# Performance work log

Measured on AMD Instinct MI355X. Metric: run time of the kernel, lower is better.

Reference implementation:

```python
import jax, jax.numpy as jnp
from jax import lax
import numpy as np


def _conv3d(x, W, b, stride=1, pad=1):
    y = lax.conv_general_dilated(x, W, (stride,) * 3, [(pad, pad)] * 3,
                                 dimension_numbers=('NCDHW', 'OIDHW', 'NCDHW'))
    return y + b[None, :, None, None, None]


def _deconv3d(x, W, b):
    # PyTorch ConvTranspose3d(k=4, s=2, p=1) == conv with lhs_dilation=2,
    # per-side pad = k-1-p = 2, spatially flipped kernel; W is (Cin, Cout, 4,4,4).
    Wf = jnp.flip(W, axis=(2, 3, 4)).transpose(1, 0, 2, 3, 4)
    y = lax.conv_general_dilated(x, Wf, (1, 1, 1), [(2, 2)] * 3,
                                 lhs_dilation=(2, 2, 2),
                                 dimension_numbers=('NCDHW', 'OIDHW', 'NCDHW'))
    return y + b[None, :, None, None, None]


def _inorm(x, eps=1e-5):
    # InstanceNorm3d (affine=False): normalize per (B, C) over spatial dims
    m = jnp.mean(x, axis=(2, 3, 4), keepdims=True)
    v = jnp.var(x, axis=(2, 3, 4), keepdims=True)
    return (x - m) * lax.rsqrt(v + eps)


def _leaky(x):
    return jnp.where(x >= 0, x, 0.1 * x)


def _cblock(x, W, b, stride=1):
    return _leaky(_inorm(_conv3d(x, W, b, stride)))


def _cost_volume(f1, f2, r=2):
    # Faithful to the original pad/mul/crop loop:
    # cost[shift][p] = mean_c f1[c, p] * f2[c, p + shift], zero-padded OOB.
    B, C, D, H, W = f1.shape
    f2p = jnp.pad(f2, ((0, 0), (0, 0), (r, r), (r, r), (r, r)))
    cv = [jnp.mean(f1 * f2p[:, :, r + v:r + v + D, r + h:r + h + H, r + d:r + d + W], axis=1)
          for v in range(-r, r + 1)
          for h in range(-r, r + 1)
          for d in range(-r, r + 1)]
    return jnp.stack(cv, axis=1)  # (B, (2r+1)^3 = 125, D, H, W)


def _warp(img, flow):
    # SpatialTransformation: dense 3D warp, trilinear sample at grid + flow,
    # coordinates clamped to the volume border.
    B, C, D, H, W = img.shape
    gd, gh, gw = jnp.meshgrid(jnp.arange(D, dtype=img.dtype),
                              jnp.arange(H, dtype=img.dtype),
                              jnp.arange(W, dtype=img.dtype), indexing='ij')
    cd = jnp.clip(gd[None] + flow[:, 0], 0.0, D - 1.0)
    ch = jnp.clip(gh[None] + flow[:, 1], 0.0, H - 1.0)
    cw = jnp.clip(gw[None] + flow[:, 2], 0.0, W - 1.0)

    def samp_b(imb, d, h, w):
        return jax.vmap(lambda c: jax.scipy.ndimage.map_coordinates(
            c, [d, h, w], order=1, mode='nearest'))(imb)

    return jax.vmap(samp_b)(img, cd, ch, cw)


def _forward(atlas, target, W_ct, b_ct, W1a, b1a, W1aa, b1aa, W1b, b1b,
             W2a, b2a, W2aa, b2aa, W2b, b2b,
             W20, b20, Wpf2, bpf2, Wd2, bd2, Wuf2, buf2,
             W10, b10, Wpf1, bpf1, Wd1, bd1, Wuf1, buf1,
             W00, b00, Wpf0, bpf0, Wd0, bd0):
    # modality='CT' (shared CT encoder), G=True, contrastive=False path
    im2 = _cblock(atlas, W_ct, b_ct, stride=2)
    im1 = _cblock(target, W_ct, b_ct, stride=2)
    c11 = _cblock(_cblock(_cblock(im1, W1a, b1a, 2), W1aa, b1aa), W1b, b1b)
    c21 = _cblock(_cblock(_cblock(im2, W1a, b1a, 2), W1aa, b1aa), W1b, b1b)
    c12 = _cblock(_cblock(_cblock(c11, W2a, b2a, 2), W2aa, b2aa), W2b, b2b)
    c22 = _cblock(_cblock(_cblock(c21, W2a, b2a, 2), W2aa, b2aa), W2b, b2b)

    x = _leaky(_cost_volume(c12, c22))
    x = _cblock(x, W20, b20)
    flow2 = _conv3d(x, Wpf2, bpf2)
    up_flow2 = _deconv3d(flow2, Wd2, bd2)
    up_feat2 = _deconv3d(x, Wuf2, buf2)

    warp1 = _warp(c21, up_flow2)
    corr1 = _leaky(_cost_volume(c11, warp1))
    x = jnp.concatenate((corr1, c11, up_flow2, up_feat2), axis=1)  # 125+16+3+3=147
    x = _cblock(x, W10, b10)
    flow1 = _conv3d(x, Wpf1, bpf1)
    up_flow1 = _deconv3d(flow1, Wd1, bd1)
    up_feat1 = _deconv3d(x, Wuf1, buf1)

    warp0 = _warp(im2, up_flow1)
    corr0 = _leaky(_cost_volume(im1, warp0))
    x = jnp.concatenate((corr0, im1, up_flow1, up_feat1), axis=1)  # 125+4+3+64=196
    x = _cblock(x, W00, b00)
    flow0 = _conv3d(x, Wpf0, bpf0)
    flow = _deconv3d(flow0, Wd0, bd0)
    return flow, c22, c12


def setup_inputs() -> dict:
    ks = jax.random.split(jax.random.key(0), 24)

    def w(i, shape):
        fan_in = int(np.prod(shape[1:]))
        return jax.random.normal(ks[i], shape, jnp.float32) * np.float32(np.sqrt(2.0 / fan_in))

    z = lambda n: jnp.zeros((n,), jnp.float32)
    S = 128
    return {
        'atlas': jax.random.normal(ks[0], (1, 1, S, S, S), jnp.float32),
        'target': jax.random.normal(ks[1], (1, 1, S, S, S), jnp.float32),
        'W_ct': w(2, (4, 1, 3, 3, 3)), 'b_ct': z(4),
        'W1a': w(3, (16, 4, 3, 3, 3)), 'b1a': z(16),
        'W1aa': w(4, (16, 16, 3, 3, 3)), 'b1aa': z(16),
        'W1b': w(5, (16, 16, 3, 3, 3)), 'b1b': z(16),
        'W2a': w(6, (32, 16, 3, 3, 3)), 'b2a': z(32),
        'W2aa': w(7, (32, 32, 3, 3, 3)), 'b2aa': z(32),
        'W2b': w(8, (32, 32, 3, 3, 3)), 'b2b': z(32),
        'W20': w(9, (32, 125, 3, 3, 3)), 'b20': z(32),
        'Wpf2': w(10, (3, 32, 3, 3, 3)) * 0.1, 'bpf2': z(3),
        'Wd2': w(11, (3, 3, 4, 4, 4)), 'bd2': z(3),
        'Wuf2': w(12, (32, 3, 4, 4, 4)), 'buf2': z(3),
        'W10': w(13, (32, 147, 3, 3, 3)), 'b10': z(32),
        'Wpf1': w(14, (3, 32, 3, 3, 3)) * 0.1, 'bpf1': z(3),
        'Wd1': w(15, (3, 3, 4, 4, 4)), 'bd1': z(3),
        'Wuf1': w(16, (32, 64, 4, 4, 4)), 'buf1': z(64),
        'W00': w(17, (32, 196, 3, 3, 3)), 'b00': z(32),
        'Wpf0': w(18, (3, 32, 3, 3, 3)) * 0.1, 'bpf0': z(3),
        'Wd0': w(19, (3, 3, 4, 4, 4)), 'bd0': z(3),
    }


def reference(atlas, target, W_ct, b_ct, W1a, b1a, W1aa, b1aa, W1b, b1b,
              W2a, b2a, W2aa, b2aa, W2b, b2b,
              W20, b20, Wpf2, bpf2, Wd2, bd2, Wuf2, buf2,
              W10, b10, Wpf1, bpf1, Wd1, bd1, Wuf1, buf1,
              W00, b00, Wpf0, bpf0, Wd0, bd0):
    return _forward(atlas, target, W_ct, b_ct, W1a, b1a, W1aa, b1aa, W1b, b1b,
                    W2a, b2a, W2aa, b2aa, W2b, b2b,
                    W20, b20, Wpf2, bpf2, Wd2, bd2, Wuf2, buf2,
                    W10, b10, Wpf1, bpf1, Wd1, bd1, Wuf1, buf1,
                    W00, b00, Wpf0, bpf0, Wd0, bd0)
```

## Files before the change

kernel.cpp:

```cpp
#include <hip/hip_runtime.h>
#include <cstddef>
#include <cstdint>

#define DIVUP(a,b) (((a)+(b)-1)/(b))

typedef __attribute__((ext_vector_type(8))) short short8;
typedef __attribute__((ext_vector_type(4))) float f32x4;

__device__ __forceinline__ ushort f2bf(float f) {
    union { float f; uint32_t u; } v; v.f = f;
    uint32_t r = v.u + 0x7fffu + ((v.u >> 16) & 1u);
    return (ushort)(r >> 16);
}

struct SwzB { int x, y, z; };
__device__ __forceinline__ SwzB swz_block() {
    int gx = gridDim.x, gy = gridDim.y;
    int n = gx * gy * gridDim.z;
    int lin = blockIdx.x + gx * (blockIdx.y + gy * blockIdx.z);
    if ((n & 7) == 0)
        lin = (lin & 7) * (n >> 3) + (lin >> 3);
    SwzB s;
    s.x = lin % gx;
    int t = lin / gx;
    s.y = t % gy;
    s.z = t / gy;
    return s;
}

template<int COUT, int STRIDE>
__global__ __launch_bounds__(256)
void conv3x3_k(const float* __restrict__ in0, const float* __restrict__ in1,
               const float* __restrict__ wgt, const float* __restrict__ bias,
               float* __restrict__ out, float* __restrict__ stats,
               int Cin, int D, int H, int W, int nz, long out_bs, int st_bs)
{
    constexpr int TD = 4, TH = 8, TW = 8;
    constexpr int ID = 2 * TD + 1, IH = 2 * TH + 1, IW = 2 * TW + 1;
    __shared__ float tile[ID * IH * IW];
    const int b = blockIdx.z / nz, zb = blockIdx.z % nz;
    const float* in = b ? in1 : in0;
    out += (long)b * out_bs;
    if (stats) stats += 2 * st_bs * b;
    const int Do = D / STRIDE, Ho = H / STRIDE, Wo = W / STRIDE;
    const int tid = threadIdx.x;
    const int tw = tid & 7, th = (tid >> 3) & 7, td = tid >> 6;
    const int ow0 = blockIdx.x * TW, oh0 = blockIdx.y * TH, od0 = zb * TD;
    const int iw0 = ow0 * STRIDE - 1, ih0 = oh0 * STRIDE - 1, id0 = od0 * STRIDE - 1;
    const size_t HWs = (size_t)H * W;

    float acc[COUT];
#pragma unroll
    for (int i = 0; i < COUT; i++) acc[i] = 0.f;

    for (int c = 0; c < Cin; ++c) {
        const float* inc = in + (size_t)c * D * HWs;
        for (int i = tid; i < ID * IH * IW; i += 256) {
            int lw = i % IW, lh = (i / IW) % IH, ld = i / (IW * IH);
            int gw = iw0 + lw, gh = ih0 + lh, gd = id0 + ld;
            float v = 0.f;
            if ((unsigned)gw < (unsigned)W && (unsigned)gh < (unsigned)H &&
                (unsigned)gd < (unsigned)D)
                v = inc[(size_t)gd * HWs + (size_t)gh * W + gw];
            tile[i] = v;
        }
        __syncthreads();
        float r[27];
        const int bd = td * STRIDE, bh = th * STRIDE, bw = tw * STRIDE;
#pragma unroll
        for (int kd = 0; kd < 3; kd++)
#pragma unroll
            for (int kh = 0; kh < 3; kh++)
#pragma unroll
                for (int kw = 0; kw < 3; kw++)
                    r[kd * 9 + kh * 3 + kw] =
                        tile[(bd + kd) * (IH * IW) + (bh + kh) * IW + (bw + kw)];
#pragma unroll
        for (int oc = 0; oc < COUT; ++oc) {
            const float* wp = wgt + ((size_t)oc * Cin + c) * 27;
            float s = 0.f;
#pragma unroll
            for (int t = 0; t < 27; t++) s = fmaf(wp[t], r[t], s);
            acc[oc] += s;
        }
        __syncthreads();
    }
    const size_t So = (size_t)Do * Ho * Wo;
    const size_t sp = (size_t)(od0 + td) * Ho * Wo + (size_t)(oh0 + th) * Wo + (ow0 + tw);
#pragma unroll
    for (int oc = 0; oc < COUT; ++oc)
        out[(size_t)oc * So + sp] = acc[oc] + bias[oc];

    if (stats) {
        __syncthreads();
        float* sm = tile;
        const int wv = tid >> 6, l = tid & 63;
#pragma unroll
        for (int oc = 0; oc < COUT; ++oc) {
            float sv = acc[oc] + bias[oc];
            float sq = sv * sv;
#pragma unroll
            for (int o = 32; o > 0; o >>= 1) {
                sv += __shfl_down(sv, o, 64);
                sq += __shfl_down(sq, o, 64);
            }
            if (l == 0) { sm[(wv * COUT + oc) * 2] = sv; sm[(wv * COUT + oc) * 2 + 1] = sq; }
        }
        __syncthreads();
        if (tid < COUT) {
            float s = 0.f, s2 = 0.f;
#pragma unroll
            for (int w = 0; w < 4; ++w) {
                s += sm[(w * COUT + tid) * 2];
                s2 += sm[(w * COUT + tid) * 2 + 1];
            }
            atomicAdd(&stats[2 * tid], s);
            atomicAdd(&stats[2 * tid + 1], s2);
        }
    }
}

template<int CP, int NF, int STRIDE, int MW, int COUTR>
__global__ __launch_bounds__(MW * 64, (STRIDE == 1 && MW == 4) ? 2 : 4)
void mconv_k(const ushort* __restrict__ xcl, const ushort* __restrict__ wp,
             const float* __restrict__ bias, float* __restrict__ outcf,
             float* __restrict__ stats, const ushort* __restrict__ zbuf,
             int D, int H, int W, int nz, long in_bs, long out_bs, int st_bs)
{
    constexpr int KC = CP / 32;
    constexpr int MF = (STRIDE == 1) ? 4 : 1;
    constexpr int TD = MW;
    constexpr int TWl = (STRIDE == 1) ? 8 : 4;
    constexpr int HD = (STRIDE == 1) ? TD + 2 : 2 * TD + 1;
    constexpr int HH = (STRIDE == 1) ? 10 : 9;
    constexpr int HWd = (STRIDE == 1) ? 10 : 9;
    constexpr int HALO = HD * HH * HWd;
    constexpr int NTH = MW * 64;
    constexpr int NIT = (HALO * 4 + NTH - 1) / NTH;
    constexpr int PITCH = (STRIDE == 1) ? 32 : 40;
    constexpr bool WLDS = (STRIDE == 1 && MW == 4);
    constexpr int LDSZ_H = (STRIDE == 1) ? NIT * NTH * 8 : HALO * 40;
    constexpr int NITW = (9 * NF * 512 + NTH * 8 - 1) / (NTH * 8);
    constexpr int LDSZ_W = NITW * NTH * 8;
    constexpr int LDS_TOT = WLDS ? LDSZ_H + 2 * LDSZ_W : LDSZ_H;
    __shared__ __align__(16) ushort lds[LDS_TOT];

    const int tid = threadIdx.x;
    const int wv = tid >> 6, l = tid & 63;
    const SwzB sb = swz_block();
    const int b = sb.z / nz, zb = sb.z % nz;
    xcl += (long)b * in_bs;
    outcf += (long)b * out_bs;
    if (stats) stats += 2 * st_bs * b;
    const int od0 = zb * TD, oh0 = sb.y * ((STRIDE == 1) ? 8 : 4),
              ow0 = sb.x * TWl;
    const int id0 = od0 * STRIDE - 1, ih0 = oh0 * STRIDE - 1, iw0 = ow0 * STRIDE - 1;

    f32x4 acc[MF][NF];
#pragma unroll
    for (int mf = 0; mf < MF; mf++)
#pragma unroll
        for (int nf = 0; nf < NF; nf++) acc[mf][nf] = f32x4{0.f, 0.f, 0.f, 0.f};

    auto woff = [&](int kc, int kd, int kh, int kw, int nf) -> size_t {
        return ((((size_t)(kc * 3 + kd) * 3 + kh) * 3 + kw) * NF + nf) << 9;
    };

    if constexpr (WLDS) {
        ushort* const hab = lds;
        ushort* const wbA = lds + LDSZ_H;
        ushort* const wbB = lds + LDSZ_H + LDSZ_W;

        auto hstage = [&](int kc) {
#pragma unroll
            for (int it = 0; it < NIT; ++it) {
                int idx = it * NTH + tid;
                int pt = idx >> 2, part = idx & 3;
                int lw = pt % HWd, lh = (pt / HWd) % HH, ld = pt / (HWd * HH);
                int gx = iw0 + lw, gy = ih0 + lh, gz = id0 + ld;
                const ushort* src = zbuf;
                if (pt < HALO && (unsigned)gx < (unsigned)W &&
                    (unsigned)gy < (unsigned)H && (unsigned)gz < (unsigned)D)
                    src = xcl + (size_t)((gz * H + gy) * W + gx) * CP + part * 8;
                __builtin_amdgcn_global_load_lds(
                    (const __attribute__((address_space(1))) uint32_t*)(src + kc * 32),
                    (__attribute__((address_space(3))) uint32_t*)
                        &hab[(size_t)(it * NTH + (wv << 6)) * 8],
                    16, 0, 0);
            }
        };
        auto wstage = [&](int kc, int kd, ushort* dst) {
#pragma unroll
            for (int it = 0; it < NITW; ++it) {
                int idx = it * NTH + tid;
                const ushort* src = (idx < 9 * NF * 64)
                    ? wp + ((size_t)(kc * 3 + kd) * 9 * NF * 512 + (size_t)idx * 8)
                    : zbuf;
                __builtin_amdgcn_global_load_lds(
                    (const __attribute__((address_space(1))) uint32_t*)src,
                    (__attribute__((address_space(3))) uint32_t*)
                        &dst[(size_t)(it * NTH + (wv << 6)) * 8],
                    16, 0, 0);
            }
        };
        auto compute = [&](int kd, const ushort* w) {
#pragma unroll
            for (int kw = 0; kw < 3; ++kw) {
                short8 af[9];
#pragma unroll
                for (int r = 0; r < 9; ++r)
                    af[r] = *reinterpret_cast<const short8*>(
                        &hab[((wv + kd) * (HH * HWd) +
                              (r + ((l >> 3) & 1)) * HWd + (l & 7) + kw) * PITCH +
                             ((l >> 4) << 3)]);
#pragma unroll
                for (int kh = 0; kh < 3; ++kh) {
                    short8 bf[NF];
#pragma unroll
                    for (int nf = 0; nf < NF; ++nf)
                        bf[nf] = *reinterpret_cast<const short8*>(
                            &w[(size_t)(((kh * 3 + kw) * NF) + nf) * 512 + (l << 3)]);
#pragma unroll
                    for (int mf = 0; mf < MF; ++mf)
#pragma unroll
                        for (int nf = 0; nf < NF; ++nf)
                            acc[mf][nf] = __builtin_amdgcn_mfma_f32_16x16x32_bf16(
                                af[2 * mf + kh], bf[nf], acc[mf][nf], 0, 0, 0);
                }
            }
        };

        for (int kc = 0; kc < KC; ++kc) {
            hstage(kc);
            wstage(kc, 0, wbA);
            __syncthreads();
            wstage(kc, 1, wbB);
            compute(0, wbA);
            __syncthreads();
            wstage(kc, 2, wbA);
            compute(1, wbB);
            __syncthreads();
            compute(2, wbA);
            __syncthreads();
        }
    } else if constexpr (STRIDE == 1) {
        for (int kc = 0; kc < KC; ++kc) {
            if (kc) __syncthreads();
#pragma unroll
            for (int it = 0; it < NIT; ++it) {
                int idx = it * NTH + tid;
                int pt = idx >> 2, part = idx & 3;
                int lw = pt % HWd, lh = (pt / HWd) % HH, ld = pt / (HWd * HH);
                int gx = iw0 + lw, gy = ih0 + lh, gz = id0 + ld;
                const ushort* src = zbuf;
                if (pt < HALO && (unsigned)gx < (unsigned)W &&
                    (unsigned)gy < (unsigned)H && (unsigned)gz < (unsigned)D)
                    src = xcl + (size_t)((gz * H + gy) * W + gx) * CP + part * 8;
                __builtin_amdgcn_global_load_lds(
                    (const __attribute__((address_space(1))) uint32_t*)(src + kc * 32),
                    (__attribute__((address_space(3))) uint32_t*)
                        &lds[(size_t)(it * NTH + (wv << 6)) * 8],
                    16, 0, 0);
            }
            __syncthreads();
#pragma unroll
            for (int kd = 0; kd < 3; ++kd) {
#pragma unroll
                for (int kw = 0; kw < 3; ++kw) {
                    short8 af[9];
#pragma unroll
                    for (int r = 0; r < 9; ++r)
                        af[r] = *reinterpret_cast<const short8*>(
                            &lds[((wv + kd) * (HH * HWd) +
                                  (r + ((l >> 3) & 1)) * HWd + (l & 7) + kw) * PITCH +
                                 ((l >> 4) << 3)]);
#pragma unroll
                    for (int kh = 0; kh < 3; ++kh) {
                        short8 bf[NF];
#pragma unroll
                        for (int nf = 0; nf < NF; ++nf)
                            bf[nf] = *reinterpret_cast<const short8*>(
                                wp + woff(kc, kd, kh, kw, nf) + (l << 3));
#pragma unroll
                        for (int mf = 0; mf < MF; ++mf)
#pragma unroll
                            for (int nf = 0; nf < NF; ++nf)
                                acc[mf][nf] = __builtin_amdgcn_mfma_f32_16x16x32_bf16(
                                    af[2 * mf + kh], bf[nf], acc[mf][nf], 0, 0, 0);
                    }
                }
            }
        }
    } else {
        uint4 v[NIT];
        auto stage = [&](int kc) {
#pragma unroll
            for (int it = 0; it < NIT; ++it) {
                int idx = it * NTH + tid;
                uint4 t = {0u, 0u, 0u, 0u};
                if (idx < HALO * 4) {
                    int pt = idx >> 2, part = idx & 3;
                    int lw = pt % HWd, lh = (pt / HWd) % HH, ld = pt / (HWd * HH);
                    int gx = iw0 + lw, gy = ih0 + lh, gz = id0 + ld;
                    if ((unsigned)gx < (unsigned)W && (unsigned)gy < (unsigned)H &&
                        (unsigned)gz < (unsigned)D)
                        t = *reinterpret_cast<const uint4*>(
                            xcl + ((size_t)((gz * H + gy) * W + gx)) * CP + kc * 32 + part * 8);
                }
                v[it] = t;
            }
        };

        stage(0);
        for (int kc = 0; kc < KC; ++kc) {
            if (kc) __syncthreads();
#pragma unroll
            for (int it = 0; it < NIT; ++it) {
                int idx = it * NTH + tid;
                if (idx < HALO * 4)
                    *reinterpret_cast<uint4*>(&lds[(idx >> 2) * PITCH + (idx & 3) * 8]) = v[it];
            }
            __syncthreads();
            if (kc + 1 < KC) stage(kc + 1);
#pragma unroll
            for (int t = 0; t < 27; ++t) {
                const int kd = t / 9, kh = (t / 3) % 3, kw = t % 3;
                short8 bf[NF];
#pragma unroll
                for (int nf = 0; nf < NF; ++nf)
                    bf[nf] = *reinterpret_cast<const short8*>(
                        wp + woff(kc, kd, kh, kw, nf) + (l << 3));
                int bw = l & 3, bh = (l >> 2) & 3;
                int p_loc = (2 * wv + kd) * (HH * HWd) + (2 * bh + kh) * HWd + (2 * bw + kw);
                short8 afs = *reinterpret_cast<const short8*>(&lds[p_loc * PITCH + ((l >> 4) << 3)]);
#pragma unroll
                for (int nf = 0; nf < NF; ++nf)
                    acc[0][nf] = __builtin_amdgcn_mfma_f32_16x16x32_bf16(
                        afs, bf[nf], acc[0][nf], 0, 0, 0);
            }
        }
    }
    const int Do = D / STRIDE, Ho = H / STRIDE, Wo = W / STRIDE;
    const size_t So = (size_t)Do * Ho * Wo;
    float ps[NF], ps2[NF];
#pragma unroll
    for (int nf = 0; nf < NF; ++nf) { ps[nf] = 0.f; ps2[nf] = 0.f; }
#pragma unroll
    for (int nf = 0; nf < NF; ++nf) {
        int oc = nf * 16 + (l & 15);
        float bv = (oc < COUTR) ? bias[oc] : 0.f;
#pragma unroll
        for (int mf = 0; mf < MF; ++mf) {
#pragma unroll
            for (int r = 0; r < 4; ++r) {
                int q = ((l >> 4) << 2) + r;
                int bw, bh;
                if (STRIDE == 1) { bw = q & 7; bh = 2 * mf + (q >> 3); }
                else             { bw = q & 3; bh = (q >> 2) & 3; }
                int p = ((od0 + wv) * Ho + (oh0 + bh)) * Wo + (ow0 + bw);
                float val = acc[mf][nf][r] + bv;
                if (oc < COUTR) {
                    outcf[(size_t)oc * So + p] = val;
                    ps[nf] += val; ps2[nf] = fmaf(val, val, ps2[nf]);
                }
            }
        }
    }
    if (stats) {
        __syncthreads();
        float* sm = (float*)lds;
#pragma unroll
        for (int nf = 0; nf < NF; ++nf) {
            float s = ps[nf], s2 = ps2[nf];
            s += __shfl_down(s, 32, 64);  s2 += __shfl_down(s2, 32, 64);
            s += __shfl_down(s, 16, 64);  s2 += __shfl_down(s2, 16, 64);
            if (l < 16) {
                sm[((wv * NF + nf) * 16 + l) * 2] = s;
                sm[((wv * NF + nf) * 16 + l) * 2 + 1] = s2;
            }
        }
        __syncthreads();
        if (tid < NF * 16) {
            int nf = tid >> 4, c = tid & 15, oc = nf * 16 + c;
            if (oc < COUTR) {
                float s = 0.f, s2 = 0.f;
#pragma unroll
                for (int w = 0; w < MW; ++w) {
                    s += sm[((w * NF + nf) * 16 + c) * 2];
                    s2 += sm[((w * NF + nf) * 16 + c) * 2 + 1];
                }
                atomicAdd(&stats[2 * oc], s);
                atomicAdd(&stats[2 * oc + 1], s2);
            }
        }
    }
}

struct WTask { const float* src; void* dst; int kind, Cin, COUT, KC, coutr, base; };
struct WTab { WTask t[17]; int n; };

__global__ __launch_bounds__(256)
void wprep_k(WTab tab)
{
    int b = blockIdx.x, ti = 0;
    for (int i = 0; i < tab.n; ++i) if (b >= tab.t[i].base) ti = i;
    const WTask tk = tab.t[ti];
    int idx = (b - tk.base) * 256 + threadIdx.x;
    if (tk.kind == 0) {
        int NF = tk.COUT >> 4;
        int tot = 27 * tk.KC * NF * 512;
        if (idx >= tot) return;
        int j = idx & 7, l = (idx >> 3) & 63;
        int g = idx >> 9;
        int nf = g % NF; g /= NF;
        int kw = g % 3; g /= 3;
        int kh = g % 3; g /= 3;
        int kd = g % 3; int kc = g / 3;
        int t = kd * 9 + kh * 3 + kw;
        int oc = nf * 16 + (l & 15);
        int c = kc * 32 + ((l >> 4) << 3) + j;
        float v = (c < tk.Cin && oc < tk.coutr)
                      ? tk.src[((size_t)oc * tk.Cin + c) * 27 + t] : 0.f;
        ((ushort*)tk.dst)[idx] = f2bf(v);
    } else if (tk.kind == 1) {
        int NF = tk.KC;
        int tot = 8 * 8 * NF * 512;
        if (idx >= tot) return;
        int j = idx & 7, l = (idx >> 3) & 63;
        int g = idx >> 9;
        int nf = g % NF; g /= NF;
        int t = g % 8; int pp = g / 8;
        int oc = nf * 16 + (l & 15);
        int c = ((l >> 4) << 3) + j;
        int kd_ = (t >> 2) & 1, kh_ = (t >> 1) & 1, kw_ = t & 1;
        int pd = (pp >> 2) & 1, ph = (pp >> 1) & 1, pw = pp & 1;
        int kd = 3 - pd - 2 * kd_, kh = 3 - ph - 2 * kh_, kw = 3 - pw - 2 * kw_;
        float v = (oc < tk.COUT)
                      ? tk.src[(size_t)(c * tk.COUT + oc) * 64 + kd * 16 + kh * 4 + kw] : 0.f;
        ((ushort*)tk.dst)[idx] = f2bf(v);
    } else {
        int tot = tk.Cin * tk.COUT * 64;
        if (idx >= tot) return;
        int k = idx & 63; int oc = (idx >> 6) % tk.COUT; int c = (idx >> 6) / tk.COUT;
        ((float*)tk.dst)[((size_t)c * 64 + k) * tk.COUT + oc] = tk.src[idx];
    }
}

template<int NF>
__global__ __launch_bounds__(256)
void mdeconv_k(const ushort* __restrict__ xcl, const ushort* __restrict__ wpd,
               const float* __restrict__ bias, ushort* __restrict__ outcl,
               int c0, int CPo, int Si)
{
    constexpr int HD = 5, HH = 9, HWd = 9, HALO = HD * HH * HWd;
    constexpr int PITCH = 32;
    __shared__ __align__(16) ushort lds[HALO * PITCH];
    const int tid = threadIdx.x, wv = tid >> 6, l = tid & 63;
    const SwzB sb = swz_block();
    const int pp = sb.z & 7, tz = sb.z >> 3;
    const int pd = (pp >> 2) & 1, ph = (pp >> 1) & 1, pw = pp & 1;
    const int oz0 = tz * 4, oy0 = sb.y * 8, ox0 = sb.x * 8;
    const int iz0 = oz0 + pd - 1, iy0 = oy0 + ph - 1, ix0 = ox0 + pw - 1;

    for (int idx = tid; idx < HALO * 4; idx += 256) {
        int pt = idx >> 2, part = idx & 3;
        int lw = pt % HWd, lh = (pt / HWd) % HH, ld = pt / (HWd * HH);
        int gx = ix0 + lw, gy = iy0 + lh, gz = iz0 + ld;
        uint4 t = {0u, 0u, 0u, 0u};
        if ((unsigned)gx < (unsigned)Si && (unsigned)gy < (unsigned)Si &&
            (unsigned)gz < (unsigned)Si)
            t = *reinterpret_cast<const uint4*>(
                xcl + ((size_t)((gz * Si + gy) * Si + gx)) * 32 + part * 8);
        *reinterpret_cast<uint4*>(&lds[pt * PITCH + part * 8]) = t;
    }
    __syncthreads();

    f32x4 acc[4][NF];
#pragma unroll
    for (int mf = 0; mf < 4; mf++)
#pragma unroll
        for (int nf = 0; nf < NF; nf++) acc[mf][nf] = f32x4{0.f, 0.f, 0.f, 0.f};

#pragma unroll
    for (int kd = 0; kd < 2; ++kd) {
#pragma unroll
        for (int kw = 0; kw < 2; ++kw) {
            short8 af[8];
#pragma unroll
            for (int r = 0; r < 8; ++r)
                af[r] = *reinterpret_cast<const short8*>(
                    &lds[((wv + kd) * (HH * HWd) + (r + ((l >> 3) & 1)) * HWd +
                          (l & 7) + kw) * PITCH + ((l >> 4) << 3)]);
#pragma unroll
            for (int kh = 0; kh < 2; ++kh) {
                const int t = kd * 4 + kh * 2 + kw;
                short8 bf[NF];
#pragma unroll
                for (int nf = 0; nf < NF; ++nf)
                    bf[nf] = *reinterpret_cast<const short8*>(
                        wpd + (((size_t)(pp * 8 + t) * NF + nf) << 9) + (l << 3));
#pragma unroll
                for (int mf = 0; mf < 4; ++mf)
#pragma unroll
                    for (int nf = 0; nf < NF; ++nf)
                        acc[mf][nf] = __builtin_amdgcn_mfma_f32_16x16x32_bf16(
                            af[2 * mf + kh], bf[nf], acc[mf][nf], 0, 0, 0);
            }
        }
    }
    const int Do = 2 * Si;
#pragma unroll
    for (int nf = 0; nf < NF; ++nf) {
        int oc = nf * 16 + (l & 15);
        float bv = bias[oc];
#pragma unroll
        for (int mf = 0; mf < 4; ++mf) {
#pragma unroll
            for (int r = 0; r < 4; ++r) {
                int q = ((l >> 4) << 2) + r;
                int bw = q & 7, bh = 2 * mf + (q >> 3);
                int oD = 2 * (oz0 + wv) + pd, oH = 2 * (oy0 + bh) + ph, oW = 2 * (ox0 + bw) + pw;
                outcl[(size_t)((oD * Do + oH) * Do + oW) * CPo + c0 + oc] =
                    f2bf(acc[mf][nf][r] + bv);
            }
        }
    }
}

template<int CIN>
__global__ __launch_bounds__(256)
void dctn_k(const float* __restrict__ in, const float* __restrict__ wt,
            const float* __restrict__ bias, float* __restrict__ outcf,
            ushort* __restrict__ outcl, int c0, int CPo, int Si)
{
    const int Do = 2 * Si;
    const size_t So = (size_t)Do * Do * Do, ni = (size_t)Si * Si * Si;
    size_t p = (size_t)blockIdx.x * 256 + threadIdx.x;
    if (p >= So) return;
    int oxW = (int)(p % Do), oyH = (int)((p / Do) % Do), ozD = (int)(p / ((size_t)Do * Do));
    int pw = oxW & 1, ph = oyH & 1, pd = ozD & 1;
    int xb = oxW >> 1, yb = oyH >> 1, zb = ozD >> 1;
    float acc[3] = {0.f, 0.f, 0.f};
    for (int c = 0; c < CIN; ++c) {
        const float* inc = in + (size_t)c * ni;
        const float* wc = wt + (size_t)c * 64 * 3;
#pragma unroll
        for (int jd = 0; jd < 2; jd++) {
            int iz = zb + pd - jd; if ((unsigned)iz >= (unsigned)Si) continue;
            int kd = 1 - pd + 2 * jd;
#pragma unroll
            for (int jh = 0; jh < 2; jh++) {
                int iy = yb + ph - jh; if ((unsigned)iy >= (unsigned)Si) continue;
                int kh = 1 - ph + 2 * jh;
#pragma unroll
                for (int jw = 0; jw < 2; jw++) {
                    int ix = xb + pw - jw; if ((unsigned)ix >= (unsigned)Si) continue;
                    int kw = 1 - pw + 2 * jw;
                    float v = inc[((size_t)iz * Si + iy) * Si + ix];
                    const float* wr = wc + (size_t)((kd * 4 + kh) * 4 + kw) * 3;
                    acc[0] = fmaf(wr[0], v, acc[0]);
                    acc[1] = fmaf(wr[1], v, acc[1]);
                    acc[2] = fmaf(wr[2], v, acc[2]);
                }
            }
        }
    }
#pragma unroll
    for (int oc = 0; oc < 3; ++oc) {
        float o = acc[oc] + bias[oc];
        if (outcf) outcf[(size_t)oc * So + p] = o;
        if (outcl) outcl[p * CPo + c0 + oc] = f2bf(o);
    }
}

__global__ __launch_bounds__(256)
void inorm_apply_k(const float* __restrict__ x, const float* __restrict__ stats,
                   float* __restrict__ y, size_t S, float invS,
                   ushort* __restrict__ ycl, int CP, int Cper, long ycl_bs)
{
    int c = blockIdx.y;
    float sum = stats[2 * c], ss = stats[2 * c + 1];
    float m = sum * invS;
    float r = rsqrtf(fmaxf(ss * invS - m * m, 0.f) + 1e-5f);
    size_t i = (size_t)blockIdx.x * 256 + threadIdx.x;
    if (i >= S) return;
    float v = (x[(size_t)c * S + i] - m) * r;
    v = v >= 0.f ? v : 0.1f * v;
    y[(size_t)c * S + i] = v;
    if (ycl) {
        int b = c / Cper, cl = c - b * Cper;
        ycl[(long)b * ycl_bs + (long)i * CP + cl] = f2bf(v);
    }
}

template<int C, int CP, int COPYC>
__global__ __launch_bounds__(256)
void costvolw_k(const float* __restrict__ f1, const float* __restrict__ f2,
                ushort* __restrict__ outcl, int D, int H, int W)
{
    const size_t S = (size_t)D * H * W;
    size_t p = (size_t)blockIdx.x * 4 + (threadIdx.x >> 6);
    if (p >= S) return;
    const int l = threadIdx.x & 63;
    int x = (int)(p % W); int y = (int)((p / W) % H); int z = (int)(p / ((size_t)W * H));
    float a[C];
#pragma unroll
    for (int c = 0; c < C; c++) a[c] = f1[(size_t)c * S + p];
    const float inv = 1.f / C;
    ushort* op = outcl + p * CP;
#pragma unroll
    for (int rep = 0; rep < 2; rep++) {
        int s = l + rep * 64;
        if (s < 125) {
            int v = s / 25 - 2, h = (s / 5) % 5 - 2, d = s % 5 - 2;
            int zz = z + v, yy = y + h, xx = x + d;
            float acc = 0.f;
            if ((unsigned)zz < (unsigned)D && (unsigned)yy < (unsigned)H &&
                (unsigned)xx < (unsigned)W) {
                size_t q = ((size_t)zz * H + yy) * (size_t)W + xx;
#pragma unroll
                for (int c = 0; c < C; c++) acc = fmaf(a[c], f2[(size_t)c * S + q], acc);
            }
            acc *= inv;
            op[s] = f2bf(acc >= 0.f ? acc : 0.1f * acc);
        }
    }
    if (COPYC && l < C)
        op[125 + l] = f2bf(f1[(size_t)l * S + p]);
}

__global__ __launch_bounds__(256)
void warp_k(const float* __restrict__ img, const float* __restrict__ flow,
            float* __restrict__ out, int C, int D, int H, int W)
{
    const size_t S = (size_t)D * H * W;
    size_t p = (size_t)blockIdx.x * 256 + threadIdx.x;
    if (p >= S) return;
    int x = (int)(p % W); int y = (int)((p / W) % H); int z = (int)(p / ((size_t)W * H));
    float cd = fminf(fmaxf((float)z + flow[p], 0.f), (float)(D - 1));
    float ch = fminf(fmaxf((float)y + flow[S + p], 0.f), (float)(H - 1));
    float cw = fminf(fmaxf((float)x + flow[2 * S + p], 0.f), (float)(W - 1));
    int d0 = (int)cd, h0 = (int)ch, w0 = (int)cw;
    float fd = cd - d0, fh = ch - h0, fw = cw - w0;
    int d1 = min(d0 + 1, D - 1), h1 = min(h0 + 1, H - 1), w1 = min(w0 + 1, W - 1);
    size_t i000 = ((size_t)d0 * H + h0) * W + w0, i001 = ((size_t)d0 * H + h0) * W + w1;
    size_t i010 = ((size_t)d0 * H + h1) * W + w0, i011 = ((size_t)d0 * H + h1) * W + w1;
    size_t i100 = ((size_t)d1 * H + h0) * W + w0, i101 = ((size_t)d1 * H + h0) * W + w1;
    size_t i110 = ((size_t)d1 * H + h1) * W + w0, i111 = ((size_t)d1 * H + h1) * W + w1;
    float w000 = (1 - fd) * (1 - fh) * (1 - fw), w001 = (1 - fd) * (1 - fh) * fw;
    float w010 = (1 - fd) * fh * (1 - fw),       w011 = (1 - fd) * fh * fw;
    float w100 = fd * (1 - fh) * (1 - fw),       w101 = fd * (1 - fh) * fw;
    float w110 = fd * fh * (1 - fw),             w111 = fd * fh * fw;
    for (int c = 0; c < C; c++) {
        const float* ic = img + (size_t)c * S;
        float v = w000 * ic[i000] + w001 * ic[i001] + w010 * ic[i010] + w011 * ic[i011]
                + w100 * ic[i100] + w101 * ic[i101] + w110 * ic[i110] + w111 * ic[i111];
        out[(size_t)c * S + p] = v;
    }
}

static void apply(hipStream_t st, float* x, int C, size_t S, const float* stats,
                  ushort* ycl, int CP, int Cper, long ycl_bs)
{
    dim3 g((unsigned)DIVUP(S, 256), C);
    inorm_apply_k<<<g, 256, 0, st>>>(x, stats, x, S, 1.0f / (float)S, ycl, CP, Cper, ycl_bs);
}

extern "C" void kernel_launch(void* const* d_in, const int* in_sizes, int n_in,
                              void* d_out, int out_size, void* d_ws, size_t ws_size,
                              hipStream_t st)
{
    (void)in_sizes; (void)n_in; (void)out_size; (void)ws_size;
    const float* atlas  = (const float*)d_in[0];
    const float* target = (const float*)d_in[1];
    const float *W_ct = (const float*)d_in[2],  *b_ct = (const float*)d_in[3];
    const float *W1a  = (const float*)d_in[4],  *b1a  = (const float*)d_in[5];
    const float *W1aa = (const float*)d_in[6],  *b1aa = (const float*)d_in[7];
    const float *W1b  = (const float*)d_in[8],  *b1b  = (const float*)d_in[9];
    const float *W2a  = (const float*)d_in[10], *b2a  = (const float*)d_in[11];
    const float *W2aa = (const float*)d_in[12], *b2aa = (const float*)d_in[13];
    const float *W2b  = (const float*)d_in[14], *b2b  = (const float*)d_in[15];
    const float *W20  = (const float*)d_in[16], *b20  = (const float*)d_in[17];
    const float *Wpf2 = (const float*)d_in[18], *bpf2 = (const float*)d_in[19];
    const float *Wd2  = (const float*)d_in[20], *bd2  = (const float*)d_in[21];
    const float *Wuf2 = (const float*)d_in[22], *buf2 = (const float*)d_in[23];
    const float *W10  = (const float*)d_in[24], *b10  = (const float*)d_in[25];
    const float *Wpf1 = (const float*)d_in[26], *bpf1 = (const float*)d_in[27];
    const float *Wd1  = (const float*)d_in[28], *bd1  = (const float*)d_in[29];
    const float *Wuf1 = (const float*)d_in[30], *buf1 = (const float*)d_in[31];
    const float *W00  = (const float*)d_in[32], *b00  = (const float*)d_in[33];
    const float *Wpf0 = (const float*)d_in[34], *bpf0 = (const float*)d_in[35];
    const float *Wd0  = (const float*)d_in[36], *bd0  = (const float*)d_in[37];

    const size_t S128 = 128u * 128 * 128, S64 = 64u * 64 * 64, S32 = 32u * 32 * 32, S16 = 16u * 16 * 16;

    char* base = (char*)d_ws;
    size_t off = 0;
    auto AF = [&](size_t n) { off = (off + 255) & ~(size_t)255; float* p = (float*)(base + off); off += n * 4; return p; };
    auto AH = [&](size_t n) { off = (off + 255) & ~(size_t)255; ushort* p = (ushort*)(base + off); off += n * 2; return p; };

    ushort* wp1a  = AH(13824);  ushort* wp1aa = AH(13824); ushort* wp1b = AH(13824);
    ushort* wp2a  = AH(27648);  ushort* wp2aa = AH(27648); ushort* wp2b = AH(27648);
    ushort* wp20  = AH(110592); ushort* wp10 = AH(138240); ushort* wp00 = AH(193536);
    ushort* wpf2  = AH(13824);  ushort* wpf1 = AH(13824);  ushort* wpf0 = AH(13824);
    ushort* wpd_uf1 = AH(131072);
    float* wt_uf2 = AF(6144);
    float* wt_d2  = AF(576);    float* wt_d1 = AF(576);    float* wt_d0 = AF(576);
    float* stats = AF(1024);
    ushort* zbuf = AH(1024);
    float* im12 = AF(8 * S64);
    float* im1 = im12; float* im2 = im12 + 4 * S64;
    float* A1   = AF(32 * S32); ushort* A1cl = AH(2 * S32 * 32);
    float* B1   = AF(32 * S32); ushort* B1cl = AH(2 * S32 * 32);
    float* c1121 = AF(32 * S32); ushort* c1121cl = AH(2 * S32 * 32);
    float* c11 = c1121; float* c21 = c1121 + 16 * S32;
    ushort* c11cl = c1121cl; ushort* c21cl = c1121cl + S32 * 32;
    float* A2   = AF(64 * S16); ushort* A2cl = AH(2 * S16 * 32);
    float* B2   = AF(64 * S16); ushort* B2cl = AH(2 * S16 * 32);
    ushort* cv2cl = AH(S16 * 128);
    float* x20  = AF(32 * S16); ushort* x20cl = AH(S16 * 32);
    float* flow2 = AF(3 * S16); float* upflow2 = AF(3 * S32);
    float* warp1 = AF(16 * S32);
    ushort* x147cl = AH(S32 * 160);
    float* x10  = AF(32 * S32); ushort* x10cl = AH(S32 * 32);
    float* flow1 = AF(3 * S32); float* upflow1 = AF(3 * S64);
    float* warp0 = AF(4 * S64);
    ushort* x196cl = AH(S64 * 224);
    float* x00  = AF(32 * S64); float* flow0 = AF(3 * S64);

    ushort* im12cl = x196cl;
    ushort* x00cl = x196cl;

    float* outF = (float*)d_out;
    float* c22o = outF + 3 * S128;
    float* c12o = c22o + 32 * S16;

    const int ST_IM=0, ST_A1=8, ST_B1=40, ST_C1=72, ST_A2=104, ST_B2=168, ST_C2=232,
              ST_X20=296, ST_X10=328, ST_X00=360;
    auto SP = [&](int o) { return stats + 2 * o; };
    hipMemsetAsync(stats, 0, 4096, st);
    hipMemsetAsync(zbuf, 0, 2048, st);

    WTab tab; int nb = 0, ti = 0;
    auto addw = [&](const float* s, void* d, int kind, int Cin, int COUT, int KC, int coutr) {
        int tot = (kind == 0) ? 27 * KC * (COUT >> 4) * 512
                 : (kind == 1) ? 8 * 8 * KC * 512 : Cin * COUT * 64;
        tab.t[ti] = WTask{s, d, kind, Cin, COUT, KC, coutr, nb};
        nb += DIVUP(tot, 256); ti++;
    };
    addw(W1a,  wp1a,  0,  4, 16, 1, 16);
    addw(W1aa, wp1aa, 0, 16, 16, 1, 16);
    addw(W1b,  wp1b,  0, 16, 16, 1, 16);
    addw(W2a,  wp2a,  0, 16, 32, 1, 32);
    addw(W2aa, wp2aa, 0, 32, 32, 1, 32);
    addw(W2b,  wp2b,  0, 32, 32, 1, 32);
    addw(W20,  wp20,  0, 125, 32, 4, 32);
    addw(W10,  wp10,  0, 147, 32, 5, 32);
    addw(W00,  wp00,  0, 196, 32, 7, 32);
    addw(Wpf2, wpf2,  0, 32, 16, 1, 3);
    addw(Wpf1, wpf1,  0, 32, 16, 1, 3);
    addw(Wpf0, wpf0,  0, 32, 16, 1, 3);
    addw(Wuf1, wpd_uf1, 1, 32, 64, 4, 64);
    addw(Wuf2, wt_uf2, 2, 32, 3, 0, 3);
    addw(Wd2,  wt_d2,  2, 3, 3, 0, 3);
    addw(Wd1,  wt_d1,  2, 3, 3, 0, 3);
    addw(Wd0,  wt_d0,  2, 3, 3, 0, 3);
    tab.n = ti;
    wprep_k<<<nb, 256, 0, st>>>(tab);

    conv3x3_k<4, 2><<<dim3(8, 8, 32), 256, 0, st>>>(target, atlas, W_ct, b_ct, im12,
                                                    SP(ST_IM), 1, 128, 128, 128,
                                                    16, (long)(4 * S64), 4);
    apply(st, im12, 8, S64, SP(ST_IM), im12cl, 32, 4, (long)(32 * S64));

    mconv_k<32, 1, 2, 4, 16><<<dim3(8, 8, 16), 256, 0, st>>>(im12cl, wp1a, b1a, A1, SP(ST_A1),
        zbuf, 64, 64, 64, 8, (long)(32 * S64), (long)(16 * S32), 16);
    apply(st, A1, 32, S32, SP(ST_A1), A1cl, 32, 16, (long)(S32 * 32));
    mconv_k<32, 1, 1, 2, 16><<<dim3(4, 4, 32), 128, 0, st>>>(A1cl, wp1aa, b1aa, B1, SP(ST_B1),
        zbuf, 32, 32, 32, 16, (long)(S32 * 32), (long)(16 * S32), 16);
    apply(st, B1, 32, S32, SP(ST_B1), B1cl, 32, 16, (long)(S32 * 32));
    mconv_k<32, 1, 1, 2, 16><<<dim3(4, 4, 32), 128, 0, st>>>(B1cl, wp1b, b1b, c1121, SP(ST_C1),
        zbuf, 32, 32, 32, 16, (long)(S32 * 32), (long)(16 * S32), 16);
    apply(st, c1121, 32, S32, SP(ST_C1), c1121cl, 32, 16, (long)(S32 * 32));

    mconv_k<32, 2, 2, 4, 32><<<dim3(4, 4, 8), 256, 0, st>>>(c1121cl, wp2a, b2a, A2, SP(ST_A2),
        zbuf, 32, 32, 32, 4, (long)(S32 * 32), (long)(32 * S16), 32);
    apply(st, A2, 64, S16, SP(ST_A2), A2cl, 32, 32, (long)(S16 * 32));
    mconv_k<32, 2, 1, 2, 32><<<dim3(2, 2, 16), 128, 0, st>>>(A2cl, wp2aa, b2aa, B2, SP(ST_B2),
        zbuf, 16, 16, 16, 8, (long)(S16 * 32), (long)(32 * S16), 32);
    apply(st, B2, 64, S16, SP(ST_B2), B2cl, 32, 32, (long)(S16 * 32));
    mconv_k<32, 2, 1, 2, 32><<<dim3(2, 2, 16), 128, 0, st>>>(B2cl, wp2b, b2b, c12o, SP(ST_C2),
        zbuf, 16, 16, 16, 8, (long)(S16 * 32), (long)(c22o - c12o), 32);
    apply(st, c12o, 32, S16, SP(ST_C2), nullptr, 0, 32, 0);
    apply(st, c22o, 32, S16, SP(ST_C2 + 32), nullptr, 0, 32, 0);

    costvolw_k<32, 128, 0><<<DIVUP(S16, 4), 256, 0, st>>>(c12o, c22o, cv2cl, 16, 16, 16);
    mconv_k<128, 2, 1, 2, 32><<<dim3(2, 2, 8), 128, 0, st>>>(cv2cl, wp20, b20, x20, SP(ST_X20),
        zbuf, 16, 16, 16, 8, 0, 0, 0);
    apply(st, x20, 32, S16, SP(ST_X20), x20cl, 32, 32, 0);
    mconv_k<32, 1, 1, 2, 3><<<dim3(2, 2, 8), 128, 0, st>>>(x20cl, wpf2, bpf2, flow2, nullptr,
        zbuf, 16, 16, 16, 8, 0, 0, 0);
    dctn_k<3><<<DIVUP(8 * S16, 256), 256, 0, st>>>(flow2, wt_d2, bd2, upflow2, x147cl, 141, 160, 16);
    dctn_k<32><<<DIVUP(8 * S16, 256), 256, 0, st>>>(x20, wt_uf2, buf2, nullptr, x147cl, 144, 160, 16);

    warp_k<<<DIVUP(S32, 256), 256, 0, st>>>(c21, upflow2, warp1, 16, 32, 32, 32);
    costvolw_k<16, 160, 1><<<DIVUP(S32, 4), 256, 0, st>>>(c11, warp1, x147cl, 32, 32, 32);
    mconv_k<160, 2, 1, 2, 32><<<dim3(4, 4, 16), 128, 0, st>>>(x147cl, wp10, b10, x10, SP(ST_X10),
        zbuf, 32, 32, 32, 16, 0, 0, 0);
    apply(st, x10, 32, S32, SP(ST_X10), x10cl, 32, 32, 0);
    mconv_k<32, 1, 1, 2, 3><<<dim3(4, 4, 16), 128, 0, st>>>(x10cl, wpf1, bpf1, flow1, nullptr,
        zbuf, 32, 32, 32, 16, 0, 0, 0);
    dctn_k<3><<<DIVUP(8 * S32, 256), 256, 0, st>>>(flow1, wt_d1, bd1, upflow1, x196cl, 129, 224, 32);
    mdeconv_k<4><<<dim3(4, 4, 64), 256, 0, st>>>(x10cl, wpd_uf1, buf1, x196cl, 132, 224, 32);

    warp_k<<<DIVUP(S64, 256), 256, 0, st>>>(im2, upflow1, warp0, 4, 64, 64, 64);
    costvolw_k<4, 224, 1><<<DIVUP(S64, 4), 256, 0, st>>>(im1, warp0, x196cl, 64, 64, 64);
    mconv_k<224, 2, 1, 4, 32><<<dim3(8, 8, 16), 256, 0, st>>>(x196cl, wp00, b00, x00, SP(ST_X00),
        zbuf, 64, 64, 64, 16, 0, 0, 0);
    apply(st, x00, 32, S64, SP(ST_X00), x00cl, 32, 32, 0);
    mconv_k<32, 1, 1, 4, 3><<<dim3(8, 8, 16), 256, 0, st>>>(x00cl, wpf0, bpf0, flow0, nullptr,
        zbuf, 64, 64, 64, 16, 0, 0, 0);
    dctn_k<3><<<DIVUP(S128, 256), 256, 0, st>>>(flow0, wt_d0, bd0, outF, nullptr, 0, 0, 64);
}
```

Measured before the change: 1.039 ms.

## Use channel-last fp32 layouts for warp and cost-volume at levels 1 and 0

```diff
diff --git a/kernel.cpp b/kernel.cpp
--- a/kernel.cpp
+++ b/kernel.cpp
@@ -576,7 +576,8 @@
 __global__ __launch_bounds__(256)
 void inorm_apply_k(const float* __restrict__ x, const float* __restrict__ stats,
                    float* __restrict__ y, size_t S, float invS,
-                   ushort* __restrict__ ycl, int CP, int Cper, long ycl_bs)
+                   ushort* __restrict__ ycl, int CP, int Cper, long ycl_bs,
+                   float* __restrict__ yclf, int CPf, int Cf)
 {
     int c = blockIdx.y;
     float sum = stats[2 * c], ss = stats[2 * c + 1];
@@ -591,6 +592,8 @@
         int b = c / Cper, cl = c - b * Cper;
         ycl[(long)b * ycl_bs + (long)i * CP + cl] = f2bf(v);
     }
+    if (yclf && c < Cf)
+        yclf[i * (size_t)CPf + c] = v;
 }
 
 template<int C, int CP, int COPYC>
@@ -629,9 +632,65 @@
         op[125 + l] = f2bf(f1[(size_t)l * S + p]);
 }
 
+template<int C, int CP, int NP>
 __global__ __launch_bounds__(256)
-void warp_k(const float* __restrict__ img, const float* __restrict__ flow,
-            float* __restrict__ out, int C, int D, int H, int W)
+void costvolcl_k(const float* __restrict__ f1cl, const float* __restrict__ f2cl,
+                 ushort* __restrict__ outcl, int D, int H, int W)
+{
+    const size_t S = (size_t)D * H * W;
+    size_t p0 = ((size_t)blockIdx.x * 4 + (threadIdx.x >> 6)) * NP;
+    if (p0 >= S) return;
+    const int l = threadIdx.x & 63;
+    float a[NP][C];
+#pragma unroll
+    for (int pp = 0; pp < NP; pp++)
+#pragma unroll
+        for (int c4 = 0; c4 < C / 4; c4++) {
+            float4 t = *reinterpret_cast<const float4*>(&f1cl[(p0 + pp) * C + c4 * 4]);
+            a[pp][c4 * 4 + 0] = t.x; a[pp][c4 * 4 + 1] = t.y;
+            a[pp][c4 * 4 + 2] = t.z; a[pp][c4 * 4 + 3] = t.w;
+        }
+    const float inv = 1.f / C;
+#pragma unroll
+    for (int rep = 0; rep < 2; rep++) {
+        int s = l + rep * 64;
+        int v = s / 25 - 2, h = (s / 5) % 5 - 2, d = s % 5 - 2;
+        bool sv = s < 125;
+#pragma unroll
+        for (int pp = 0; pp < NP; pp++) {
+            size_t p = p0 + pp;
+            int x = (int)(p % W), y = (int)((p / W) % H), z = (int)(p / ((size_t)W * H));
+            int zz = z + v, yy = y + h, xx = x + d;
+            float acc = 0.f;
+            if (sv && (unsigned)zz < (unsigned)D && (unsigned)yy < (unsigned)H &&
+                (unsigned)xx < (unsigned)W) {
+                size_t q = ((size_t)zz * H + yy) * (size_t)W + xx;
+#pragma unroll
+                for (int c4 = 0; c4 < C / 4; c4++) {
+                    float4 b = *reinterpret_cast<const float4*>(&f2cl[q * C + c4 * 4]);
+                    acc = fmaf(a[pp][c4 * 4 + 0], b.x, acc);
+                    acc = fmaf(a[pp][c4 * 4 + 1], b.y, acc);
+                    acc = fmaf(a[pp][c4 * 4 + 2], b.z, acc);
+                    acc = fmaf(a[pp][c4 * 4 + 3], b.w, acc);
+                }
+            }
+            if (sv) {
+                acc *= inv;
+                outcl[p * CP + s] = f2bf(acc >= 0.f ? acc : 0.1f * acc);
+            }
+        }
+    }
+    if (l < C) {
+#pragma unroll
+        for (int pp = 0; pp < NP; pp++)
+            outcl[(p0 + pp) * CP + 125 + l] = f2bf(f1cl[(p0 + pp) * C + l]);
+    }
+}
+
+template<int C>
+__global__ __launch_bounds__(256)
+void warpcl_k(const float* __restrict__ img, const float* __restrict__ flow,
+              float* __restrict__ outcl, int D, int H, int W)
 {
     const size_t S = (size_t)D * H * W;
     size_t p = (size_t)blockIdx.x * 256 + threadIdx.x;
@@ -651,19 +710,27 @@
     float w010 = (1 - fd) * fh * (1 - fw),       w011 = (1 - fd) * fh * fw;
     float w100 = fd * (1 - fh) * (1 - fw),       w101 = fd * (1 - fh) * fw;
     float w110 = fd * fh * (1 - fw),             w111 = fd * fh * fw;
-    for (int c = 0; c < C; c++) {
-        const float* ic = img + (size_t)c * S;
-        float v = w000 * ic[i000] + w001 * ic[i001] + w010 * ic[i010] + w011 * ic[i011]
-                + w100 * ic[i100] + w101 * ic[i101] + w110 * ic[i110] + w111 * ic[i111];
-        out[(size_t)c * S + p] = v;
+#pragma unroll
+    for (int c4 = 0; c4 < C / 4; c4++) {
+        float4 r;
+        float* rr = reinterpret_cast<float*>(&r);
+#pragma unroll
+        for (int j = 0; j < 4; j++) {
+            const float* ic = img + (size_t)(c4 * 4 + j) * S;
+            rr[j] = w000 * ic[i000] + w001 * ic[i001] + w010 * ic[i010] + w011 * ic[i011]
+                  + w100 * ic[i100] + w101 * ic[i101] + w110 * ic[i110] + w111 * ic[i111];
+        }
+        *reinterpret_cast<float4*>(&outcl[p * C + c4 * 4]) = r;
     }
 }
 
 static void apply(hipStream_t st, float* x, int C, size_t S, const float* stats,
-                  ushort* ycl, int CP, int Cper, long ycl_bs)
+                  ushort* ycl, int CP, int Cper, long ycl_bs,
+                  float* yclf = nullptr, int CPf = 0, int Cf = 0)
 {
     dim3 g((unsigned)DIVUP(S, 256), C);
-    inorm_apply_k<<<g, 256, 0, st>>>(x, stats, x, S, 1.0f / (float)S, ycl, CP, Cper, ycl_bs);
+    inorm_apply_k<<<g, 256, 0, st>>>(x, stats, x, S, 1.0f / (float)S, ycl, CP, Cper, ycl_bs,
+                                     yclf, CPf, Cf);
 }
 
 extern "C" void kernel_launch(void* const* d_in, const int* in_sizes, int n_in,
@@ -710,21 +777,22 @@
     ushort* zbuf = AH(1024);
     float* im12 = AF(8 * S64);
     float* im1 = im12; float* im2 = im12 + 4 * S64;
+    float* im1clf = AF(4 * S64);
+    float* warp0clf = AF(4 * S64);
+    float* c11clf = AF(16 * S32);
+    float* warp1clf = AF(16 * S32);
     float* A1   = AF(32 * S32); ushort* A1cl = AH(2 * S32 * 32);
     float* B1   = AF(32 * S32); ushort* B1cl = AH(2 * S32 * 32);
     float* c1121 = AF(32 * S32); ushort* c1121cl = AH(2 * S32 * 32);
     float* c11 = c1121; float* c21 = c1121 + 16 * S32;
-    ushort* c11cl = c1121cl; ushort* c21cl = c1121cl + S32 * 32;
     float* A2   = AF(64 * S16); ushort* A2cl = AH(2 * S16 * 32);
     float* B2   = AF(64 * S16); ushort* B2cl = AH(2 * S16 * 32);
     ushort* cv2cl = AH(S16 * 128);
     float* x20  = AF(32 * S16); ushort* x20cl = AH(S16 * 32);
     float* flow2 = AF(3 * S16); float* upflow2 = AF(3 * S32);
-    float* warp1 = AF(16 * S32);
     ushort* x147cl = AH(S32 * 160);
     float* x10  = AF(32 * S32); ushort* x10cl = AH(S32 * 32);
     float* flow1 = AF(3 * S32); float* upflow1 = AF(3 * S64);
-    float* warp0 = AF(4 * S64);
     ushort* x196cl = AH(S64 * 224);
     float* x00  = AF(32 * S64); float* flow0 = AF(3 * S64);
 
@@ -771,7 +839,7 @@
     conv3x3_k<4, 2><<<dim3(8, 8, 32), 256, 0, st>>>(target, atlas, W_ct, b_ct, im12,
                                                     SP(ST_IM), 1, 128, 128, 128,
                                                     16, (long)(4 * S64), 4);
-    apply(st, im12, 8, S64, SP(ST_IM), im12cl, 32, 4, (long)(32 * S64));
+    apply(st, im12, 8, S64, SP(ST_IM), im12cl, 32, 4, (long)(32 * S64), im1clf, 4, 4);
 
     mconv_k<32, 1, 2, 4, 16><<<dim3(8, 8, 16), 256, 0, st>>>(im12cl, wp1a, b1a, A1, SP(ST_A1),
         zbuf, 64, 64, 64, 8, (long)(32 * S64), (long)(16 * S32), 16);
@@ -781,7 +849,7 @@
     apply(st, B1, 32, S32, SP(ST_B1), B1cl, 32, 16, (long)(S32 * 32));
     mconv_k<32, 1, 1, 2, 16><<<dim3(4, 4, 32), 128, 0, st>>>(B1cl, wp1b, b1b, c1121, SP(ST_C1),
         zbuf, 32, 32, 32, 16, (long)(S32 * 32), (long)(16 * S32), 16);
-    apply(st, c1121, 32, S32, SP(ST_C1), c1121cl, 32, 16, (long)(S32 * 32));
+    apply(st, c1121, 32, S32, SP(ST_C1), c1121cl, 32, 16, (long)(S32 * 32), c11clf, 16, 16);
 
     mconv_k<32, 2, 2, 4, 32><<<dim3(4, 4, 8), 256, 0, st>>>(c1121cl, wp2a, b2a, A2, SP(ST_A2),
         zbuf, 32, 32, 32, 4, (long)(S32 * 32), (long)(32 * S16), 32);
@@ -803,8 +871,9 @@
     dctn_k<3><<<DIVUP(8 * S16, 256), 256, 0, st>>>(flow2, wt_d2, bd2, upflow2, x147cl, 141, 160, 16);
     dctn_k<32><<<DIVUP(8 * S16, 256), 256, 0, st>>>(x20, wt_uf2, buf2, nullptr, x147cl, 144, 160, 16);
 
-    warp_k<<<DIVUP(S32, 256), 256, 0, st>>>(c21, upflow2, warp1, 16, 32, 32, 32);
-    costvolw_k<16, 160, 1><<<DIVUP(S32, 4), 256, 0, st>>>(c11, warp1, x147cl, 32, 32, 32);
+    warpcl_k<16><<<DIVUP(S32, 256), 256, 0, st>>>(c21, upflow2, warp1clf, 32, 32, 32);
+    costvolcl_k<16, 160, 2><<<(unsigned)(S32 / 8), 256, 0, st>>>(c11clf, warp1clf, x147cl,
+                                                                 32, 32, 32);
     mconv_k<160, 2, 1, 2, 32><<<dim3(4, 4, 16), 128, 0, st>>>(x147cl, wp10, b10, x10, SP(ST_X10),
         zbuf, 32, 32, 32, 16, 0, 0, 0);
     apply(st, x10, 32, S32, SP(ST_X10), x10cl, 32, 32, 0);
@@ -813,8 +882,9 @@
     dctn_k<3><<<DIVUP(8 * S32, 256), 256, 0, st>>>(flow1, wt_d1, bd1, upflow1, x196cl, 129, 224, 32);
     mdeconv_k<4><<<dim3(4, 4, 64), 256, 0, st>>>(x10cl, wpd_uf1, buf1, x196cl, 132, 224, 32);
 
-    warp_k<<<DIVUP(S64, 256), 256, 0, st>>>(im2, upflow1, warp0, 4, 64, 64, 64);
-    costvolw_k<4, 224, 1><<<DIVUP(S64, 4), 256, 0, st>>>(im1, warp0, x196cl, 64, 64, 64);
+    warpcl_k<4><<<DIVUP(S64, 256), 256, 0, st>>>(im2, upflow1, warp0clf, 64, 64, 64);
+    costvolcl_k<4, 224, 4><<<(unsigned)(S64 / 16), 256, 0, st>>>(im1clf, warp0clf, x196cl,
+                                                                 64, 64, 64);
     mconv_k<224, 2, 1, 4, 32><<<dim3(8, 8, 16), 256, 0, st>>>(x196cl, wp00, b00, x00, SP(ST_X00),
         zbuf, 64, 64, 64, 16, 0, 0, 0);
     apply(st, x00, 32, S64, SP(ST_X00), x00cl, 32, 32, 0);
```

Result: faster. 922.9 us (-11.2%).
